# Kernel tuning notes

Measured on AMD Instinct MI355X. Metric: run time of the kernel, lower is better.

The kernel has to match this reference:

```python
import jax, jax.numpy as jnp
import numpy as np

EPS = 1e-5

def setup_inputs() -> dict:
    key = jax.random.key(0)
    ks = jax.random.split(key, 16)
    B, C, F, T = 8, 32, 32, 4000
    Ch = C // 2  # 16
    inp = {}
    inp["x"] = jax.random.normal(ks[0], (B, C, F, T), dtype=jnp.float32)
    # q/k/v 1x1 conv blocks stacked along leading axis: order [q, k, v]
    inp["qkv_W"] = jax.random.normal(ks[1], (3, Ch, C), dtype=jnp.float32) * 0.1
    inp["qkv_b"] = jax.random.normal(ks[2], (3, Ch), dtype=jnp.float32) * 0.1
    inp["qkv_gamma"] = 1.0 + 0.1 * jax.random.normal(ks[3], (3, Ch), dtype=jnp.float32)
    inp["qkv_beta"] = 0.1 * jax.random.normal(ks[4], (3, Ch), dtype=jnp.float32)
    inp["qkv_mean"] = 0.1 * jax.random.normal(ks[5], (3, Ch), dtype=jnp.float32)
    inp["qkv_var"] = jax.random.uniform(ks[6], (3, Ch), dtype=jnp.float32, minval=0.5, maxval=1.5)
    inp["qkv_alpha"] = jnp.full((3,), 0.25, dtype=jnp.float32)  # PReLU slopes
    # enc 1x1 conv block: Ch -> C
    inp["enc_W"] = jax.random.normal(ks[7], (C, Ch), dtype=jnp.float32) * 0.1
    inp["enc_b"] = jax.random.normal(ks[8], (C,), dtype=jnp.float32) * 0.1
    inp["enc_gamma"] = 1.0 + 0.1 * jax.random.normal(ks[9], (C,), dtype=jnp.float32)
    inp["enc_beta"] = 0.1 * jax.random.normal(ks[10], (C,), dtype=jnp.float32)
    inp["enc_mean"] = 0.1 * jax.random.normal(ks[11], (C,), dtype=jnp.float32)
    inp["enc_var"] = jax.random.uniform(ks[12], (C,), dtype=jnp.float32, minval=0.5, maxval=1.5)
    inp["enc_alpha"] = jnp.asarray(0.25, dtype=jnp.float32)
    return inp


def reference(x, qkv_W, qkv_b, qkv_gamma, qkv_beta, qkv_mean, qkv_var, qkv_alpha,
              enc_W, enc_b, enc_gamma, enc_beta, enc_mean, enc_var, enc_alpha):
    B, C, F, T = x.shape
    Ch = C // 2
    D = Ch * F  # flattened token feature dim
    # --- q/k/v ConvBlocks (1x1 conv + inference BN + PReLU), batched over qkv axis ---
    h = jnp.einsum('noi,bift->nboft', qkv_W, x) + qkv_b[:, None, :, None, None]
    inv = (qkv_gamma / jnp.sqrt(qkv_var + EPS))[:, None, :, None, None]
    h = (h - qkv_mean[:, None, :, None, None]) * inv + qkv_beta[:, None, :, None, None]
    h = jnp.where(h > 0, h, qkv_alpha[:, None, None, None, None] * h)
    q, k, v = h[0], h[1], h[2]  # each [B, Ch, F, T]

    def to_tokens(z):
        return z.reshape(B, D, T).transpose(0, 2, 1)  # [B, T, D]

    scale = float(np.sqrt(D))
    qm = to_tokens(q)
    km = to_tokens(k) / scale
    vm = to_tokens(v)
    # sigmoid-gated attention (no softmax normalization)
    mask = jax.nn.sigmoid(jnp.einsum('btd,bsd->bts', qm, km))  # [B, T, T]
    sa = jnp.einsum('bts,bsd->btd', mask, vm)                   # [B, T, D]
    sa = sa.transpose(0, 2, 1).reshape(B, Ch, F, T)
    # --- enc ConvBlock + residual ---
    e = jnp.einsum('oi,bift->boft', enc_W, sa) + enc_b[None, :, None, None]
    einv = (enc_gamma / jnp.sqrt(enc_var + EPS))[None, :, None, None]
    e = (e - enc_mean[None, :, None, None]) * einv + enc_beta[None, :, None, None]
    e = jnp.where(e > 0, e, enc_alpha * e)
    return e + x
```

## Files before the change

### kernel.cpp

```cpp
#include <hip/hip_runtime.h>

typedef __attribute__((ext_vector_type(8))) short bf16x8;
typedef __attribute__((ext_vector_type(4))) float floatx4;
typedef __attribute__((ext_vector_type(4))) unsigned int uintx4;

#define EPSF 1e-5f
#define RS512 0.04419417382415922f

__device__ __forceinline__ unsigned short f2bf(float f) {
  unsigned int u = __float_as_uint(f);
  u += 0x7fffu + ((u >> 16) & 1u);
  return (unsigned short)(u >> 16);
}

union BFrag { bf16x8 v; int i[4]; unsigned short s[8]; };

__device__ __forceinline__ void gll16(const void* g, void* l) {
  __builtin_amdgcn_global_load_lds(
      (__attribute__((address_space(1))) void*)g,
      (__attribute__((address_space(3))) void*)l, 16, 0, 0);
}

__global__ __launch_bounds__(512) void qkv_kernel(
    const float* __restrict__ x,
    const float* __restrict__ Wq, const float* __restrict__ bq,
    const float* __restrict__ gq, const float* __restrict__ beq,
    const float* __restrict__ mq, const float* __restrict__ vq,
    const float* __restrict__ aq,
    unsigned short* __restrict__ Q, unsigned short* __restrict__ K,
    unsigned short* __restrict__ V) {
  const int b = blockIdx.y;
  const int t0 = blockIdx.x << 4;
  const int tid = threadIdx.x;

  __shared__ unsigned short xs[16 * 1032];
  __shared__ float sW[1584];
  __shared__ float sB[48];
  __shared__ unsigned short vsm[512 * 18];

  for (int idx = tid; idx < 1536; idx += 512) {
    int n = idx >> 9, ch = (idx >> 5) & 15;
    float inv = gq[n * 16 + ch] * rsqrtf(vq[n * 16 + ch] + EPSF);
    if (n == 1) inv *= RS512;
    sW[n * 528 + ch * 33 + (idx & 31)] = Wq[idx] * inv;
  }
  if (tid < 48) {
    int n = tid >> 4;
    float inv = gq[tid] * rsqrtf(vq[tid] + EPSF);
    float bb = (bq[tid] - mq[tid]) * inv + beq[tid];
    if (n == 1) bb *= RS512;
    sB[tid] = bb;
  }
  {
    int tq = tid & 3, rq = tid >> 2;
    const float* xb = x + (size_t)b * 1024 * 4000 + t0 + (tq << 2);
    for (int rr = rq; rr < 1024; rr += 128) {
      float4 f = *(const float4*)(xb + (size_t)rr * 4000);
      xs[(tq * 4 + 0) * 1032 + rr] = f2bf(f.x);
      xs[(tq * 4 + 1) * 1032 + rr] = f2bf(f.y);
      xs[(tq * 4 + 2) * 1032 + rr] = f2bf(f.z);
      xs[(tq * 4 + 3) * 1032 + rr] = f2bf(f.w);
    }
  }
  __syncthreads();

  const int lane = tid & 63, w = tid >> 6;
  const int c = lane & 15, qd = lane >> 4;
  const int wg = w >> 2;
  const int lt = (w & 3) * 4 + qd;
  const int t = t0 + lt;
  const int f0 = (c & 3) * 8;
  const unsigned short* xrow = xs + lt * 1032;
  const float aQ = aq[0], aK = aq[1], aV = aq[2];

  for (int p = 0; p < 2; ++p) {
    const int pp = p + (wg << 1);
    const int ch = (c >> 2) + (pp << 2);
    float acq[8], ack[8], acv[8];
#pragma unroll
    for (int j = 0; j < 8; ++j) {
      acq[j] = sB[ch]; ack[j] = sB[16 + ch]; acv[j] = sB[32 + ch];
    }
    const float* wqp = sW + ch * 33;
    const float* wkp = sW + 528 + ch * 33;
    const float* wvp = sW + 1056 + ch * 33;
    for (int i = 0; i < 32; ++i) {
      BFrag xf;
      xf.v = *(const bf16x8*)(xrow + i * 32 + f0);
      float wqi = wqp[i], wki = wkp[i], wvi2 = wvp[i];
#pragma unroll
      for (int j = 0; j < 8; ++j) {
        float xv = __uint_as_float((unsigned int)xf.s[j] << 16);
        acq[j] += wqi * xv; ack[j] += wki * xv; acv[j] += wvi2 * xv;
      }
    }
    unsigned int qw[4], kw[4];
#pragma unroll
    for (int j2 = 0; j2 < 4; ++j2) {
      float q0 = acq[2 * j2], q1 = acq[2 * j2 + 1];
      q0 = q0 > 0.f ? q0 : aQ * q0; q1 = q1 > 0.f ? q1 : aQ * q1;
      qw[j2] = (unsigned int)f2bf(q0) | ((unsigned int)f2bf(q1) << 16);
      float k0 = ack[2 * j2], k1 = ack[2 * j2 + 1];
      k0 = k0 > 0.f ? k0 : aK * k0; k1 = k1 > 0.f ? k1 : aK * k1;
      kw[j2] = (unsigned int)f2bf(k0) | ((unsigned int)f2bf(k1) << 16);
    }
    const int d0 = (pp << 7) + (c << 3);
    uintx4 qv, kv;
    qv[0] = qw[0]; qv[1] = qw[1]; qv[2] = qw[2]; qv[3] = qw[3];
    kv[0] = kw[0]; kv[1] = kw[1]; kv[2] = kw[2]; kv[3] = kw[3];
    *(uintx4*)(Q + (size_t)(b * 4000 + t) * 512 + d0) = qv;
    *(uintx4*)(K + (size_t)(b * 4000 + t) * 512 + d0) = kv;
#pragma unroll
    for (int j = 0; j < 8; ++j) {
      float v0 = acv[j];
      v0 = v0 > 0.f ? v0 : aV * v0;
      vsm[(d0 + j) * 18 + lt] = f2bf(v0);
    }
  }
  __syncthreads();
  {
    const int st = t0 >> 5;
    const int toff = t0 & 16;
    unsigned short* vt = V + ((size_t)(b * 125 + st) * 512) * 32 + toff;
    for (int i = tid; i < 4096; i += 512) {
      int d = i >> 3, u = i & 7;
      unsigned int w2 = *(unsigned int*)&vsm[d * 18 + 2 * u];
      ((unsigned int*)(vt + d * 32))[u] = w2;
    }
  }
}

__global__ __launch_bounds__(512, 2) void attn_kernel(
    const float* __restrict__ x,
    const float* __restrict__ encW, const float* __restrict__ encb,
    const float* __restrict__ encg, const float* __restrict__ encbe,
    const float* __restrict__ encm, const float* __restrict__ encv,
    const float* __restrict__ enca,
    const unsigned short* __restrict__ Q, const unsigned short* __restrict__ K,
    const unsigned short* __restrict__ V, float* __restrict__ out) {
  const int tid = threadIdx.x;
  const int lane = tid & 63;
  const int w = tid >> 6;
  const int b = blockIdx.x >> 5;
  const int bt0 = (blockIdx.x & 31) << 7;
  const int t0 = bt0 + (w << 4);
  const bool active = t0 < 4000;
  const int c = lane & 15, qd = lane >> 4;

  __shared__ __align__(16) unsigned char smem[142336];
  unsigned short* Ksb = (unsigned short*)smem;
  unsigned short* Vsb = Ksb + 2 * 16640;
  unsigned short* Pb = Vsb + 2 * 16384;
  float* Eb = (float*)smem;

  for (int i = tid; i < 2560; i += 512) ((unsigned int*)Pb)[i] = 0u;

  bf16x8 qf[16];
  {
    const int tq = active ? t0 : 0;
    const unsigned short* qp = Q + (size_t)(b * 4000 + tq + c) * 512 + qd * 8;
#pragma unroll
    for (int ks = 0; ks < 16; ++ks) qf[ks] = *(const bf16x8*)(qp + ks * 32);
  }

  floatx4 acc[4][8];
#pragma unroll
  for (int m = 0; m < 4; ++m)
#pragma unroll
    for (int q2 = 0; q2 < 8; ++q2) {
      acc[m][q2][0] = 0.f; acc[m][q2][1] = 0.f;
      acc[m][q2][2] = 0.f; acc[m][q2][3] = 0.f;
    }

  const unsigned short* Kb = K + (size_t)b * 4000 * 512;
  const unsigned short* Vb = V + (size_t)b * 125 * 16384;

  const int r0 = w << 2;
  const int lby = lane * 8;
  const int vmask = ((lane >> 2) & 7) ^ ((lane >> 4) & 1);
  const int vsw = (lane ^ vmask) << 3;

  auto stage = [&](int buf, int it) {
    const unsigned short* kg = Kb + (size_t)it * 16384;
    const unsigned short* vg = Vb + (size_t)it * 16384;
    unsigned short* kd = Ksb + buf * 16640;
    unsigned short* vd = Vsb + buf * 16384;
#pragma unroll
    for (int r = 0; r < 4; ++r) {
      gll16(kg + (size_t)((r0 + r) << 9) + lby, kd + (r0 + r) * 520);
      gll16(vg + (size_t)((r0 + r) << 9) + vsw, vd + ((r0 + r) << 9));
    }
  };

  stage(0, 0);
  int cur = 0;

#pragma unroll 1
  for (int it = 0; it < 125; ++it) {
    asm volatile("s_waitcnt vmcnt(0)" ::: "memory");
    __syncthreads();
    if (it + 1 < 125) stage(cur ^ 1, it + 1);

    if (active) {
      floatx4 sa0, sa1;
      sa0[0] = sa0[1] = sa0[2] = sa0[3] = 0.f;
      sa1 = sa0;
      const unsigned short* kp = Ksb + cur * 16640 + c * 520 + qd * 8;
      __builtin_amdgcn_s_setprio(1);
#pragma unroll
      for (int ks = 0; ks < 16; ++ks) {
        bf16x8 k0 = *(const bf16x8*)(kp + ks * 32);
        bf16x8 k1 = *(const bf16x8*)(kp + 16 * 520 + ks * 32);
        sa0 = __builtin_amdgcn_mfma_f32_16x16x32_bf16(k0, qf[ks], sa0, 0, 0, 0);
        sa1 = __builtin_amdgcn_mfma_f32_16x16x32_bf16(k1, qf[ks], sa1, 0, 0, 0);
      }
      __builtin_amdgcn_s_setprio(0);
      float p0 = __builtin_amdgcn_rcpf(1.f + __expf(-sa0[0]));
      float p1 = __builtin_amdgcn_rcpf(1.f + __expf(-sa0[1]));
      float p2 = __builtin_amdgcn_rcpf(1.f + __expf(-sa0[2]));
      float p3 = __builtin_amdgcn_rcpf(1.f + __expf(-sa0[3]));
      float p4 = __builtin_amdgcn_rcpf(1.f + __expf(-sa1[0]));
      float p5 = __builtin_amdgcn_rcpf(1.f + __expf(-sa1[1]));
      float p6 = __builtin_amdgcn_rcpf(1.f + __expf(-sa1[2]));
      float p7 = __builtin_amdgcn_rcpf(1.f + __expf(-sa1[3]));
      unsigned short* pw = Pb + ((w << 4) + c) * 40 + (qd << 2);
      uint2 pa, pb2;
      pa.x = (unsigned int)f2bf(p0) | ((unsigned int)f2bf(p1) << 16);
      pa.y = (unsigned int)f2bf(p2) | ((unsigned int)f2bf(p3) << 16);
      pb2.x = (unsigned int)f2bf(p4) | ((unsigned int)f2bf(p5) << 16);
      pb2.y = (unsigned int)f2bf(p6) | ((unsigned int)f2bf(p7) << 16);
      *(uint2*)pw = pa;
      *(uint2*)(pw + 16) = pb2;
    }
    __syncthreads();

    {
      const unsigned short* vp =
          Vsb + cur * 16384 + ((((c << 2) | qd) ^ (c & 7)) << 3);
      bf16x8 vf[4];
#pragma unroll
      for (int m = 0; m < 4; ++m)
        vf[m] = *(const bf16x8*)(vp + ((r0 + m) << 9));
      __builtin_amdgcn_s_setprio(1);
#pragma unroll
      for (int h = 0; h < 2; ++h) {
        bf16x8 pf[4];
#pragma unroll
        for (int q2 = 0; q2 < 4; ++q2)
          pf[q2] = *(const bf16x8*)(Pb + ((((h << 2) | q2) << 4) + c) * 40 +
                                    (qd << 3));
#pragma unroll
        for (int m = 0; m < 4; ++m)
#pragma unroll
          for (int q2 = 0; q2 < 4; ++q2)
            acc[m][(h << 2) | q2] = __builtin_amdgcn_mfma_f32_16x16x32_bf16(
                vf[m], pf[q2], acc[m][(h << 2) | q2], 0, 0, 0);
      }
      __builtin_amdgcn_s_setprio(0);
    }
    cur ^= 1;
  }

  __syncthreads();

  const float ealpha = enca[0];
#pragma unroll
  for (int rnd = 0; rnd < 2; ++rnd) {
#pragma unroll
    for (int m = 0; m < 4; ++m)
#pragma unroll
      for (int q2 = 0; q2 < 4; ++q2)
        *(floatx4*)&Eb[((q2 << 4) + c) * 516 + (w << 6) + (m << 4) +
                       (qd << 2)] = acc[m][(rnd << 2) | q2];
    __syncthreads();
    if ((w >> 2) == rnd && active) {
      const float* er = Eb + (((w & 3) << 4) + c) * 516;
#pragma unroll
      for (int hi = 0; hi < 2; ++hi) {
        floatx4 sh[16];
#pragma unroll
        for (int i = 0; i < 16; ++i)
          sh[i] = *(const floatx4*)&er[(i << 5) + (hi << 4) + (qd << 2)];
#pragma unroll 1
        for (int o = 0; o < 32; ++o) {
          float inv = encg[o] * rsqrtf(encv[o] + EPSF);
          float bfo = (encb[o] - encm[o]) * inv + encbe[o];
          float e0 = 0.f, e1 = 0.f, e2 = 0.f, e3 = 0.f;
#pragma unroll
          for (int i = 0; i < 16; ++i) {
            float wi = encW[(o << 4) + i];
            e0 += wi * sh[i][0]; e1 += wi * sh[i][1];
            e2 += wi * sh[i][2]; e3 += wi * sh[i][3];
          }
          float ee[4] = {e0, e1, e2, e3};
#pragma unroll
          for (int rr = 0; rr < 4; ++rr) {
            float e = ee[rr] * inv + bfo;
            e = e > 0.f ? e : ealpha * e;
            int fq = (qd << 2) + rr + (hi << 4);
            size_t idx = ((size_t)((b << 5) + o) * 32 + fq) * 4000 + t0 + c;
            out[idx] = e + x[idx];
          }
        }
      }
    }
    __syncthreads();
  }
}

extern "C" void kernel_launch(void* const* d_in, const int* in_sizes, int n_in,
                              void* d_out, int out_size, void* d_ws,
                              size_t ws_size, hipStream_t stream) {
  const float* x = (const float*)d_in[0];
  unsigned short* Q = (unsigned short*)d_ws;
  unsigned short* K = Q + (size_t)8 * 4000 * 512;
  unsigned short* V = K + (size_t)8 * 4000 * 512;

  dim3 g1(250, 8);
  qkv_kernel<<<g1, 512, 0, stream>>>(
      x, (const float*)d_in[1], (const float*)d_in[2], (const float*)d_in[3],
      (const float*)d_in[4], (const float*)d_in[5], (const float*)d_in[6],
      (const float*)d_in[7], Q, K, V);

  attn_kernel<<<dim3(256), 512, 0, stream>>>(
      x, (const float*)d_in[8], (const float*)d_in[9], (const float*)d_in[10],
      (const float*)d_in[11], (const float*)d_in[12], (const float*)d_in[13],
      (const float*)d_in[14], Q, K, V, (float*)d_out);
}
```

Before: 641.0 us.

## Restructure attention loop to 64-key tiles with single-buffered K/V staging

```diff
diff --git a/kernel.cpp b/kernel.cpp
--- a/kernel.cpp
+++ b/kernel.cpp
@@ -141,27 +141,17 @@
   const int tid = threadIdx.x;
   const int lane = tid & 63;
   const int w = tid >> 6;
-  const int b = blockIdx.x >> 5;
-  const int bt0 = (blockIdx.x & 31) << 7;
+  const int b = blockIdx.x & 7;
+  const int bt0 = (blockIdx.x >> 3) << 7;
   const int t0 = bt0 + (w << 4);
   const bool active = t0 < 4000;
   const int c = lane & 15, qd = lane >> 4;
 
-  __shared__ __align__(16) unsigned char smem[142336];
+  __shared__ __align__(16) unsigned char smem[150528];
   unsigned short* Ksb = (unsigned short*)smem;
-  unsigned short* Vsb = Ksb + 2 * 16640;
-  unsigned short* Pb = Vsb + 2 * 16384;
+  unsigned short* Vsb = Ksb + 64 * 520;
+  unsigned short* Pb = Vsb + 512 * 64;
   float* Eb = (float*)smem;
-
-  for (int i = tid; i < 2560; i += 512) ((unsigned int*)Pb)[i] = 0u;
-
-  bf16x8 qf[16];
-  {
-    const int tq = active ? t0 : 0;
-    const unsigned short* qp = Q + (size_t)(b * 4000 + tq + c) * 512 + qd * 8;
-#pragma unroll
-    for (int ks = 0; ks < 16; ++ks) qf[ks] = *(const bf16x8*)(qp + ks * 32);
-  }
 
   floatx4 acc[4][8];
 #pragma unroll
@@ -172,93 +162,126 @@
       acc[m][q2][2] = 0.f; acc[m][q2][3] = 0.f;
     }
 
+  const unsigned short* Qg = Q + (size_t)b * 4000 * 512;
   const unsigned short* Kb = K + (size_t)b * 4000 * 512;
   const unsigned short* Vb = V + (size_t)b * 125 * 16384;
 
-  const int r0 = w << 2;
-  const int lby = lane * 8;
-  const int vmask = ((lane >> 2) & 7) ^ ((lane >> 4) & 1);
-  const int vsw = (lane ^ vmask) << 3;
-
-  auto stage = [&](int buf, int it) {
-    const unsigned short* kg = Kb + (size_t)it * 16384;
-    const unsigned short* vg = Vb + (size_t)it * 16384;
-    unsigned short* kd = Ksb + buf * 16640;
-    unsigned short* vd = Vsb + buf * 16384;
-#pragma unroll
-    for (int r = 0; r < 4; ++r) {
-      gll16(kg + (size_t)((r0 + r) << 9) + lby, kd + (r0 + r) * 520);
-      gll16(vg + (size_t)((r0 + r) << 9) + vsw, vd + ((r0 + r) << 9));
+  const int qg = w & 3, sg = w >> 2;
+  int q0i = bt0 + qg * 32 + c;      if (q0i > 3999) q0i = 3999;
+  int q1i = bt0 + qg * 32 + 16 + c; if (q1i > 3999) q1i = 3999;
+  const unsigned short* qp0 = Qg + (size_t)q0i * 512 + qd * 8;
+  const unsigned short* qp1 = Qg + (size_t)q1i * 512 + qd * 8;
+  const unsigned short* kp0 = Ksb + (sg * 32 + c) * 520 + qd * 8;
+  const unsigned short* kp1 = kp0 + 16 * 520;
+
+  const int vkl = (lane & 7) ^ ((lane >> 3) & 7);
+  const int vth = vkl >> 2;
+  const int vro = lane >> 3;
+  const int vco = (vkl & 3) * 8;
+
+  unsigned short* pw0 = Pb + (qg * 32 + c) * 72 + sg * 32 + qd * 4;
+
+  auto stageK = [&](int it) {
+    const int rr = w << 3;
+#pragma unroll
+    for (int j = 0; j < 8; ++j) {
+      int t = it * 64 + rr + j; if (t > 3999) t = 3999;
+      gll16(Kb + (size_t)t * 512 + lane * 8, Ksb + (rr + j) * 520);
     }
   };
-
-  stage(0, 0);
-  int cur = 0;
+  auto stageV = [&](int it) {
+    int ti = it * 2 + vth; if (ti > 124) ti = 124;
+    const unsigned short* src = Vb + (size_t)ti * 16384 + vro * 32 + vco;
+    unsigned short* dst = Vsb + (w << 12);
+#pragma unroll
+    for (int j = 0; j < 8; ++j)
+      gll16(src + ((w << 3) + j) * 256, dst + (j << 9));
+  };
+
+  stageK(0);
 
 #pragma unroll 1
-  for (int it = 0; it < 125; ++it) {
+  for (int it = 0; it < 63; ++it) {
     asm volatile("s_waitcnt vmcnt(0)" ::: "memory");
     __syncthreads();
-    if (it + 1 < 125) stage(cur ^ 1, it + 1);
-
-    if (active) {
-      floatx4 sa0, sa1;
-      sa0[0] = sa0[1] = sa0[2] = sa0[3] = 0.f;
-      sa1 = sa0;
-      const unsigned short* kp = Ksb + cur * 16640 + c * 520 + qd * 8;
-      __builtin_amdgcn_s_setprio(1);
-#pragma unroll
-      for (int ks = 0; ks < 16; ++ks) {
-        bf16x8 k0 = *(const bf16x8*)(kp + ks * 32);
-        bf16x8 k1 = *(const bf16x8*)(kp + 16 * 520 + ks * 32);
-        sa0 = __builtin_amdgcn_mfma_f32_16x16x32_bf16(k0, qf[ks], sa0, 0, 0, 0);
-        sa1 = __builtin_amdgcn_mfma_f32_16x16x32_bf16(k1, qf[ks], sa1, 0, 0, 0);
+
+    floatx4 s00, s01, s10, s11;
+    s00[0] = s00[1] = s00[2] = s00[3] = 0.f;
+    s01 = s00; s10 = s00; s11 = s00;
+    __builtin_amdgcn_s_setprio(1);
+#pragma unroll
+    for (int ks = 0; ks < 4; ++ks) {
+      bf16x8 a0 = *(const bf16x8*)(qp0 + ks * 32);
+      bf16x8 a1 = *(const bf16x8*)(qp1 + ks * 32);
+      bf16x8 k0 = *(const bf16x8*)(kp0 + ks * 32);
+      bf16x8 k1 = *(const bf16x8*)(kp1 + ks * 32);
+      s00 = __builtin_amdgcn_mfma_f32_16x16x32_bf16(k0, a0, s00, 0, 0, 0);
+      s01 = __builtin_amdgcn_mfma_f32_16x16x32_bf16(k1, a0, s01, 0, 0, 0);
+      s10 = __builtin_amdgcn_mfma_f32_16x16x32_bf16(k0, a1, s10, 0, 0, 0);
+      s11 = __builtin_amdgcn_mfma_f32_16x16x32_bf16(k1, a1, s11, 0, 0, 0);
+    }
+    __builtin_amdgcn_s_setprio(0);
+    __builtin_amdgcn_sched_barrier(0);
+    stageV(it);
+    __builtin_amdgcn_sched_barrier(0);
+    __builtin_amdgcn_s_setprio(1);
+#pragma unroll 4
+    for (int ks = 4; ks < 16; ++ks) {
+      bf16x8 a0 = *(const bf16x8*)(qp0 + ks * 32);
+      bf16x8 a1 = *(const bf16x8*)(qp1 + ks * 32);
+      bf16x8 k0 = *(const bf16x8*)(kp0 + ks * 32);
+      bf16x8 k1 = *(const bf16x8*)(kp1 + ks * 32);
+      s00 = __builtin_amdgcn_mfma_f32_16x16x32_bf16(k0, a0, s00, 0, 0, 0);
+      s01 = __builtin_amdgcn_mfma_f32_16x16x32_bf16(k1, a0, s01, 0, 0, 0);
+      s10 = __builtin_amdgcn_mfma_f32_16x16x32_bf16(k0, a1, s10, 0, 0, 0);
+      s11 = __builtin_amdgcn_mfma_f32_16x16x32_bf16(k1, a1, s11, 0, 0, 0);
+    }
+    __builtin_amdgcn_s_setprio(0);
+
+    {
+      const bool sval = (it < 62) || (sg == 0);
+      floatx4 sa[4] = {s00, s01, s10, s11};
+      uint2 z[4];
+#pragma unroll
+      for (int fgi = 0; fgi < 4; ++fgi) {
+        float p0 = __builtin_amdgcn_rcpf(1.f + __expf(-sa[fgi][0]));
+        float p1 = __builtin_amdgcn_rcpf(1.f + __expf(-sa[fgi][1]));
+        float p2 = __builtin_amdgcn_rcpf(1.f + __expf(-sa[fgi][2]));
+        float p3 = __builtin_amdgcn_rcpf(1.f + __expf(-sa[fgi][3]));
+        z[fgi].x = sval ? ((unsigned int)f2bf(p0) | ((unsigned int)f2bf(p1) << 16)) : 0u;
+        z[fgi].y = sval ? ((unsigned int)f2bf(p2) | ((unsigned int)f2bf(p3) << 16)) : 0u;
       }
-      __builtin_amdgcn_s_setprio(0);
-      float p0 = __builtin_amdgcn_rcpf(1.f + __expf(-sa0[0]));
-      float p1 = __builtin_amdgcn_rcpf(1.f + __expf(-sa0[1]));
-      float p2 = __builtin_amdgcn_rcpf(1.f + __expf(-sa0[2]));
-      float p3 = __builtin_amdgcn_rcpf(1.f + __expf(-sa0[3]));
-      float p4 = __builtin_amdgcn_rcpf(1.f + __expf(-sa1[0]));
-      float p5 = __builtin_amdgcn_rcpf(1.f + __expf(-sa1[1]));
-      float p6 = __builtin_amdgcn_rcpf(1.f + __expf(-sa1[2]));
-      float p7 = __builtin_amdgcn_rcpf(1.f + __expf(-sa1[3]));
-      unsigned short* pw = Pb + ((w << 4) + c) * 40 + (qd << 2);
-      uint2 pa, pb2;
-      pa.x = (unsigned int)f2bf(p0) | ((unsigned int)f2bf(p1) << 16);
-      pa.y = (unsigned int)f2bf(p2) | ((unsigned int)f2bf(p3) << 16);
-      pb2.x = (unsigned int)f2bf(p4) | ((unsigned int)f2bf(p5) << 16);
-      pb2.y = (unsigned int)f2bf(p6) | ((unsigned int)f2bf(p7) << 16);
-      *(uint2*)pw = pa;
-      *(uint2*)(pw + 16) = pb2;
-    }
+      *(uint2*)pw0 = z[0];
+      *(uint2*)(pw0 + 16) = z[1];
+      *(uint2*)(pw0 + 16 * 72) = z[2];
+      *(uint2*)(pw0 + 16 * 72 + 16) = z[3];
+    }
+
+    asm volatile("s_waitcnt vmcnt(0)" ::: "memory");
     __syncthreads();
-
-    {
-      const unsigned short* vp =
-          Vsb + cur * 16384 + ((((c << 2) | qd) ^ (c & 7)) << 3);
-      bf16x8 vf[4];
-#pragma unroll
-      for (int m = 0; m < 4; ++m)
-        vf[m] = *(const bf16x8*)(vp + ((r0 + m) << 9));
-      __builtin_amdgcn_s_setprio(1);
-#pragma unroll
-      for (int h = 0; h < 2; ++h) {
-        bf16x8 pf[4];
-#pragma unroll
-        for (int q2 = 0; q2 < 4; ++q2)
-          pf[q2] = *(const bf16x8*)(Pb + ((((h << 2) | q2) << 4) + c) * 40 +
-                                    (qd << 3));
-#pragma unroll
-        for (int m = 0; m < 4; ++m)
-#pragma unroll
-          for (int q2 = 0; q2 < 4; ++q2)
-            acc[m][(h << 2) | q2] = __builtin_amdgcn_mfma_f32_16x16x32_bf16(
-                vf[m], pf[q2], acc[m][(h << 2) | q2], 0, 0, 0);
+    if (it + 1 < 63) stageK(it + 1);
+
+    bf16x8 vf[4][2];
+#pragma unroll
+    for (int md = 0; md < 4; ++md) {
+      const int r = (w << 6) + (md << 4) + c;
+#pragma unroll
+      for (int k2 = 0; k2 < 2; ++k2)
+        vf[md][k2] = *(const bf16x8*)(
+            Vsb + (((r << 3) + (((k2 << 2) + qd) ^ (r & 7))) << 3));
+    }
+    __builtin_amdgcn_s_setprio(1);
+#pragma unroll
+    for (int k2 = 0; k2 < 2; ++k2)
+#pragma unroll
+      for (int q2 = 0; q2 < 8; ++q2) {
+        bf16x8 pf = *(const bf16x8*)(Pb + ((q2 << 4) + c) * 72 + (k2 << 5) + (qd << 3));
+#pragma unroll
+        for (int md = 0; md < 4; ++md)
+          acc[md][q2] = __builtin_amdgcn_mfma_f32_16x16x32_bf16(
+              vf[md][k2], pf, acc[md][q2], 0, 0, 0);
       }
-      __builtin_amdgcn_s_setprio(0);
-    }
-    cur ^= 1;
+    __builtin_amdgcn_s_setprio(0);
   }
 
   __syncthreads();
```

New measurement: 975.1 us. 1.52x slower.

## Compute QKV 1x1 projection with bf16 MFMA using split hi/lo weights

Applied to the files above, without the earlier changes.

```diff
diff --git a/kernel.cpp b/kernel.cpp
--- a/kernel.cpp
+++ b/kernel.cpp
@@ -33,16 +33,17 @@
   const int t0 = blockIdx.x << 4;
   const int tid = threadIdx.x;
 
-  __shared__ unsigned short xs[16 * 1032];
-  __shared__ float sW[1584];
+  __shared__ __align__(16) unsigned char smem[53760];
+  unsigned short* xs2 = (unsigned short*)smem;
+  float* sWf = (float*)(smem + 41472);
+  unsigned short* sWA = (unsigned short*)(smem + 47616);
   __shared__ float sB[48];
-  __shared__ unsigned short vsm[512 * 18];
 
   for (int idx = tid; idx < 1536; idx += 512) {
     int n = idx >> 9, ch = (idx >> 5) & 15;
     float inv = gq[n * 16 + ch] * rsqrtf(vq[n * 16 + ch] + EPSF);
     if (n == 1) inv *= RS512;
-    sW[n * 528 + ch * 33 + (idx & 31)] = Wq[idx] * inv;
+    sWf[idx] = Wq[idx] * inv;
   }
   if (tid < 48) {
     int n = tid >> 4;
@@ -56,75 +57,101 @@
     const float* xb = x + (size_t)b * 1024 * 4000 + t0 + (tq << 2);
     for (int rr = rq; rr < 1024; rr += 128) {
       float4 f = *(const float4*)(xb + (size_t)rr * 4000);
-      xs[(tq * 4 + 0) * 1032 + rr] = f2bf(f.x);
-      xs[(tq * 4 + 1) * 1032 + rr] = f2bf(f.y);
-      xs[(tq * 4 + 2) * 1032 + rr] = f2bf(f.z);
-      xs[(tq * 4 + 3) * 1032 + rr] = f2bf(f.w);
+      const int cc = rr >> 5, fch = rr & 31;
+      unsigned short* dst = xs2 + fch * 648 + (tq << 2) * 40 + cc;
+      dst[0] = f2bf(f.x);
+      dst[40] = f2bf(f.y);
+      dst[80] = f2bf(f.z);
+      dst[120] = f2bf(f.w);
+    }
+  }
+  __syncthreads();
+
+  for (int a = tid; a < 3072; a += 512) {
+    int j = a & 7, l = (a >> 3) & 63, slot = a >> 9;
+    int n = slot >> 1, hl = slot & 1;
+    int ch = l & 15, cc = ((l >> 4) << 3) + j;
+    float wf = sWf[(n * 16 + ch) * 32 + cc];
+    unsigned short hi = f2bf(wf);
+    if (hl) {
+      float hif = __uint_as_float((unsigned int)hi << 16);
+      sWA[a] = f2bf(wf - hif);
+    } else {
+      sWA[a] = hi;
     }
   }
   __syncthreads();
 
   const int lane = tid & 63, w = tid >> 6;
-  const int c = lane & 15, qd = lane >> 4;
-  const int wg = w >> 2;
-  const int lt = (w & 3) * 4 + qd;
-  const int t = t0 + lt;
-  const int f0 = (c & 3) * 8;
-  const unsigned short* xrow = xs + lt * 1032;
+  const int tl = lane & 15, qd = lane >> 4;
   const float aQ = aq[0], aK = aq[1], aV = aq[2];
 
-  for (int p = 0; p < 2; ++p) {
-    const int pp = p + (wg << 1);
-    const int ch = (c >> 2) + (pp << 2);
-    float acq[8], ack[8], acv[8];
-#pragma unroll
-    for (int j = 0; j < 8; ++j) {
-      acq[j] = sB[ch]; ack[j] = sB[16 + ch]; acv[j] = sB[32 + ch];
-    }
-    const float* wqp = sW + ch * 33;
-    const float* wkp = sW + 528 + ch * 33;
-    const float* wvp = sW + 1056 + ch * 33;
-    for (int i = 0; i < 32; ++i) {
-      BFrag xf;
-      xf.v = *(const bf16x8*)(xrow + i * 32 + f0);
-      float wqi = wqp[i], wki = wkp[i], wvi2 = wvp[i];
-#pragma unroll
-      for (int j = 0; j < 8; ++j) {
-        float xv = __uint_as_float((unsigned int)xf.s[j] << 16);
-        acq[j] += wqi * xv; ack[j] += wki * xv; acv[j] += wvi2 * xv;
+  bf16x8 Af[3][2];
+#pragma unroll
+  for (int n = 0; n < 3; ++n)
+#pragma unroll
+    for (int hl = 0; hl < 2; ++hl)
+      Af[n][hl] = *(const bf16x8*)(sWA + ((((n << 1) + hl) << 6) + lane) * 8);
+
+  floatx4 acc[3][4];
+#pragma unroll
+  for (int n = 0; n < 3; ++n)
+#pragma unroll
+    for (int ff = 0; ff < 4; ++ff) {
+      acc[n][ff][0] = 0.f; acc[n][ff][1] = 0.f;
+      acc[n][ff][2] = 0.f; acc[n][ff][3] = 0.f;
+    }
+
+#pragma unroll
+  for (int ff = 0; ff < 4; ++ff) {
+    const int f = (w << 2) + ff;
+    bf16x8 xb = *(const bf16x8*)(xs2 + f * 648 + tl * 40 + (qd << 3));
+#pragma unroll
+    for (int n = 0; n < 3; ++n) {
+      acc[n][ff] = __builtin_amdgcn_mfma_f32_16x16x32_bf16(Af[n][0], xb, acc[n][ff], 0, 0, 0);
+      acc[n][ff] = __builtin_amdgcn_mfma_f32_16x16x32_bf16(Af[n][1], xb, acc[n][ff], 0, 0, 0);
+    }
+  }
+  __syncthreads();
+
+  unsigned short* oQ = (unsigned short*)smem;
+  unsigned short* oK = oQ + 16 * 520;
+  unsigned short* oV = oK + 16 * 520;
+#pragma unroll
+  for (int n = 0; n < 3; ++n) {
+    const float sl = (n == 0) ? aQ : ((n == 1) ? aK : aV);
+#pragma unroll
+    for (int ff = 0; ff < 4; ++ff) {
+      const int f = (w << 2) + ff;
+#pragma unroll
+      for (int rr = 0; rr < 4; ++rr) {
+        const int ch = (qd << 2) + rr;
+        float v = acc[n][ff][rr] + sB[n * 16 + ch];
+        v = v > 0.f ? v : sl * v;
+        unsigned short us = f2bf(v);
+        const int d = (ch << 5) + f;
+        if (n == 0) oQ[tl * 520 + d] = us;
+        else if (n == 1) oK[tl * 520 + d] = us;
+        else oV[d * 18 + tl] = us;
       }
     }
-    unsigned int qw[4], kw[4];
-#pragma unroll
-    for (int j2 = 0; j2 < 4; ++j2) {
-      float q0 = acq[2 * j2], q1 = acq[2 * j2 + 1];
-      q0 = q0 > 0.f ? q0 : aQ * q0; q1 = q1 > 0.f ? q1 : aQ * q1;
-      qw[j2] = (unsigned int)f2bf(q0) | ((unsigned int)f2bf(q1) << 16);
-      float k0 = ack[2 * j2], k1 = ack[2 * j2 + 1];
-      k0 = k0 > 0.f ? k0 : aK * k0; k1 = k1 > 0.f ? k1 : aK * k1;
-      kw[j2] = (unsigned int)f2bf(k0) | ((unsigned int)f2bf(k1) << 16);
-    }
-    const int d0 = (pp << 7) + (c << 3);
-    uintx4 qv, kv;
-    qv[0] = qw[0]; qv[1] = qw[1]; qv[2] = qw[2]; qv[3] = qw[3];
-    kv[0] = kw[0]; kv[1] = kw[1]; kv[2] = kw[2]; kv[3] = kw[3];
-    *(uintx4*)(Q + (size_t)(b * 4000 + t) * 512 + d0) = qv;
-    *(uintx4*)(K + (size_t)(b * 4000 + t) * 512 + d0) = kv;
-#pragma unroll
-    for (int j = 0; j < 8; ++j) {
-      float v0 = acv[j];
-      v0 = v0 > 0.f ? v0 : aV * v0;
-      vsm[(d0 + j) * 18 + lt] = f2bf(v0);
-    }
-  }
-  __syncthreads();
+  }
+  __syncthreads();
+
+  for (int i = tid; i < 1024; i += 512) {
+    int t = i >> 6, u = i & 63;
+    *(uintx4*)(Q + (size_t)(b * 4000 + t0 + t) * 512 + u * 8) =
+        *(const uintx4*)(oQ + t * 520 + u * 8);
+    *(uintx4*)(K + (size_t)(b * 4000 + t0 + t) * 512 + u * 8) =
+        *(const uintx4*)(oK + t * 520 + u * 8);
+  }
   {
     const int st = t0 >> 5;
     const int toff = t0 & 16;
     unsigned short* vt = V + ((size_t)(b * 125 + st) * 512) * 32 + toff;
     for (int i = tid; i < 4096; i += 512) {
       int d = i >> 3, u = i & 7;
-      unsigned int w2 = *(unsigned int*)&vsm[d * 18 + 2 * u];
+      unsigned int w2 = *(unsigned int*)&oV[d * 18 + 2 * u];
       ((unsigned int*)(vt + d * 32))[u] = w2;
     }
   }
```

Measured after the change: 626.9 us. -2.2%, faster.
